# Optimization experiments

Hardware: AMD Instinct MI355X
Metric: run time of the kernel (lower is better)

Reference implementation:

```python
import jax, jax.numpy as jnp
import numpy as np

N, M, NBR = 20000, 12, 64
AF, ORIG, H, B, K = 256, 92, 256, 200, 50
N_CONV = 3
EPS = 1e-5


def _bn_train(x, gamma, beta):
    mu = x.mean(0)
    var = x.var(0)  # biased, matches torch BN normalization in train mode
    return (x - mu) * jax.lax.rsqrt(var + EPS) * gamma + beta


def _conv_layer(atom_in, nbr_fea, nbr_idx, w1, b1, w2, b2, gamma, beta):
    n, m = nbr_idx.shape
    m1 = m // 2
    atom_nbr = atom_in[nbr_idx]                     # [N, M, AF]
    atom_u = jnp.broadcast_to(atom_in[:, None, :], (n, m1, atom_in.shape[-1]))
    an1, an2 = atom_nbr[:, :m1], atom_nbr[:, m1:]
    nf1, nf2 = nbr_fea[:, :m1], nbr_fea[:, m1:]
    u1 = jnp.concatenate([atom_u, an1, nf1], axis=2)  # [N, M1, 2*AF+NBR]
    u2 = jnp.concatenate([atom_u, an2, nf2], axis=2)
    g1 = jax.nn.relu(jnp.einsum('nmf,fo->nmo', u1, w1) + b1)
    g2 = jax.nn.softplus(jnp.einsum('nmf,fo->nmo', u2, w1) + b1)
    nbr_sumed = g1.sum(1) + g2.sum(1)               # sum over all M neighbors, [N, 2*AF]
    nbr_sumed = nbr_sumed @ w2 + b2                 # [N, AF]
    nbr_sumed = _bn_train(nbr_sumed, gamma, beta)
    return jax.nn.softplus(atom_in + nbr_sumed)


def setup_inputs() -> dict:
    key = jax.random.key(0)
    ks = jax.random.split(key, 16)
    inp = {
        'atom_fea': jax.random.normal(ks[0], (N, ORIG), jnp.float32),
        'nbr_fea': jax.random.normal(ks[1], (N, M, NBR), jnp.float32),
        'nbr_fea_idx': jax.random.randint(ks[2], (N, M), 0, N),
        'M1_index': jax.random.randint(ks[3], (B * K,), 0, N),
        'seg_ids': jnp.repeat(jnp.arange(B), K),
        'm2_fea': jax.random.normal(ks[4], (B, 4), jnp.float32),
        'emb_w': jax.random.normal(ks[5], (ORIG, AF), jnp.float32) * 0.05,
        'emb_b': jnp.zeros((AF,), jnp.float32),
        'w1': jax.random.normal(ks[6], (N_CONV, 2 * AF + NBR, 2 * AF), jnp.float32) * 0.05,
        'b1': jnp.zeros((N_CONV, 2 * AF), jnp.float32),
        'w2': jax.random.normal(ks[7], (N_CONV, 2 * AF, AF), jnp.float32) * 0.05,
        'b2': jnp.zeros((N_CONV, AF), jnp.float32),
        'gamma': jnp.ones((N_CONV, AF), jnp.float32),
        'beta': jnp.zeros((N_CONV, AF), jnp.float32),
        'fc_w': jax.random.normal(ks[8], (AF + 4, H), jnp.float32) * 0.05,
        'fc_b': jnp.zeros((H,), jnp.float32),
        'out_w': jax.random.normal(ks[9], (H, 1), jnp.float32) * 0.05,
        'out_b': jnp.zeros((1,), jnp.float32),
    }
    return inp


def reference(atom_fea, nbr_fea, nbr_fea_idx, M1_index, seg_ids, m2_fea,
              emb_w, emb_b, w1, b1, w2, b2, gamma, beta,
              fc_w, fc_b, out_w, out_b):
    x = jax.nn.softplus(atom_fea @ emb_w + emb_b)           # [N, AF]
    for i in range(N_CONV):
        x = _conv_layer(x, nbr_fea, nbr_fea_idx, w1[i], b1[i], w2[i], b2[i], gamma[i], beta[i])
    m1_fea = x[M1_index]                                    # [B*K, AF]
    sums = jax.ops.segment_sum(m1_fea, seg_ids, num_segments=B)
    counts = jax.ops.segment_sum(jnp.ones((m1_fea.shape[0], 1), m1_fea.dtype), seg_ids, num_segments=B)
    crys = sums / counts                                    # per-crystal mean, [B, AF]
    crys = jnp.concatenate([crys, m2_fea], axis=1)          # [B, AF+4]
    h = jax.nn.softplus(jax.nn.softplus(crys) @ fc_w + fc_b)
    out = h @ out_w + out_b                                 # [B, 1]
    return out
```

## Files before the change

### kernel.cpp

```cpp
#include <hip/hip_runtime.h>
#include <hip/hip_bf16.h>


#define N_ATOM 20000
#define AF     256
#define F2     512
#define ORIG   92
#define ORIG_P 96
#define BB     200
#define KK     50
#define BN_EPS 1e-5f
#define ZPS    132

#define OFF_B1   0
#define OFF_B2   1536
#define OFF_GAM  2304
#define OFF_BET  3072
#define OFF_EMBB 3840
#define OFF_FCB  4096
#define OFF_FCW  4352
#define OFF_OW   70912
#define OFF_OB   71168
#define OFF_M2   71169
#define N_SMALL  71969

#define S_AF   (N_ATOM * ORIG_P)
#define S_EMB  (AF * ORIG_P)
#define S_W12  (3 * 1024 * 256)
#define S_W1F  (3 * 512 * 64)
#define S_W2   (3 * AF * F2)
#define S_SM   N_SMALL
#define S_TOT  (S_AF + S_EMB + S_W12 + S_W1F + S_W2 + S_SM)

using bf16x8 = __attribute__((ext_vector_type(8))) short;
using f32x4  = __attribute__((ext_vector_type(4))) float;

__device__ __forceinline__ float bf2f(__hip_bfloat16 v) { return __bfloat162float(v); }
__device__ __forceinline__ __hip_bfloat16 f2bf(float v) { return __float2bfloat16(v); }
__device__ __forceinline__ unsigned short f2bfbits(float f) {
    unsigned u = __float_as_uint(f);
    u += 0x7fffu + ((u >> 16) & 1u);
    return (unsigned short)(u >> 16);
}
__device__ __forceinline__ float bfbits2f(unsigned short u) {
    return __uint_as_float(((unsigned)u) << 16);
}
__device__ __forceinline__ unsigned pack2bf(float lo, float hi) {
    unsigned ul = __float_as_uint(lo);
    unsigned uh = __float_as_uint(hi);
    ul += 0x7fffu + ((ul >> 16) & 1u);
    uh += 0x7fffu + ((uh >> 16) & 1u);
    return __builtin_amdgcn_perm(uh, ul, 0x07060302u);
}
__device__ __forceinline__ float softplus_f(float x) {
    return fmaxf(x, 0.f) + __logf(1.f + __expf(-fabsf(x)));
}
__device__ __forceinline__ float ld_any(const void* p, long idx, bool isf32) {
    return isf32 ? ((const float*)p)[idx] : bf2f(((const __hip_bfloat16*)p)[idx]);
}

__global__ void detect_dtype(const unsigned* __restrict__ gamma_raw,
                             unsigned* __restrict__ flag) {
    unsigned u = gamma_raw[0];
    flag[0] = ((u & 0xFFFFu) == 0u) ? 1u : 0u;
}

__global__ __launch_bounds__(256) void prep_nf(const void* __restrict__ nf,
                                               const unsigned* __restrict__ dflag,
                                               unsigned* __restrict__ out) {
    bool isf32 = dflag[0] != 0u;
    int idx = blockIdx.x * 256 + threadIdx.x;
    if (idx >= N_ATOM * 12 * 64 / 4) return;
    if (isf32) {
        float4 v = ((const float4*)nf)[idx];
        out[idx * 2]     = pack2bf(v.x, v.y);
        out[idx * 2 + 1] = pack2bf(v.z, v.w);
    } else {
        ((uint2*)out)[idx] = ((const uint2*)nf)[idx];
    }
}

__global__ __launch_bounds__(256)
void prep_all(const void* af, const void* emb_w, const void* w1, const void* w2,
              const void* b1, const void* b2, const void* gam, const void* bet,
              const void* embb, const void* fcb, const void* fcw,
              const void* ow, const void* ob, const void* m2,
              const unsigned* __restrict__ dflag,
              __hip_bfloat16* __restrict__ af_pad, __hip_bfloat16* __restrict__ embT,
              __hip_bfloat16* __restrict__ w1T2, __hip_bfloat16* __restrict__ w1Tf,
              __hip_bfloat16* __restrict__ w2T, __hip_bfloat16* __restrict__ smalls) {
    bool isf32 = dflag[0] != 0u;
    int i = blockIdx.x * 256 + threadIdx.x;
    if (i < S_AF) {
        int r = i / ORIG_P, k = i - r * ORIG_P;
        af_pad[i] = (k < ORIG) ? f2bf(ld_any(af, (long)r * ORIG + k, isf32)) : f2bf(0.f);
        return;
    }
    i -= S_AF;
    if (i < S_EMB) {
        int n = i / ORIG_P, k = i - n * ORIG_P;
        embT[i] = (k < ORIG) ? f2bf(ld_any(emb_w, (long)k * AF + n, isf32)) : f2bf(0.f);
        return;
    }
    i -= S_EMB;
    if (i < S_W12) {
        int l = i / (1024 * 256); int rem = i - l * (1024 * 256);
        int c = rem / 256, k = rem - c * 256;
        long src = (c < 512) ? ((long)(l * 576 + k) * F2 + c)
                             : ((long)(l * 576 + 256 + k) * F2 + (c - 512));
        w1T2[i] = f2bf(ld_any(w1, src, isf32));
        return;
    }
    i -= S_W12;
    if (i < S_W1F) {
        int l = i / (512 * 64); int rem = i - l * (512 * 64);
        int c = rem / 64, k = rem - c * 64;
        w1Tf[i] = f2bf(ld_any(w1, (long)(l * 576 + 512 + k) * F2 + c, isf32));
        return;
    }
    i -= S_W1F;
    if (i < S_W2) {
        int l = i / (AF * F2); int rem = i - l * (AF * F2);
        int n = rem / F2, k = rem - n * F2;
        w2T[i] = f2bf(ld_any(w2, (long)(l * F2 + k) * AF + n, isf32));
        return;
    }
    i -= S_W2;
    if (i >= S_SM) return;
    float v;
    if      (i < OFF_B2)   v = ld_any(b1,   i - OFF_B1,  isf32);
    else if (i < OFF_GAM)  v = ld_any(b2,   i - OFF_B2,  isf32);
    else if (i < OFF_BET)  v = ld_any(gam,  i - OFF_GAM, isf32);
    else if (i < OFF_EMBB) v = ld_any(bet,  i - OFF_BET, isf32);
    else if (i < OFF_FCB)  v = ld_any(embb, i - OFF_EMBB,isf32);
    else if (i < OFF_OW)   v = (i < OFF_FCW) ? ld_any(fcb, i - OFF_FCB, isf32)
                                             : ld_any(fcw, i - OFF_FCW, isf32);
    else if (i < OFF_OB)   v = ld_any(ow,   i - OFF_OW,  isf32);
    else if (i < OFF_M2)   v = ld_any(ob,   i - OFF_OB,  isf32);
    else                   v = ld_any(m2,   i - OFF_M2,  isf32);
    smalls[i] = f2bf(v);
}

template <bool OUT_BF16>
__global__ __launch_bounds__(256)
void gemm_kernel(const __hip_bfloat16* __restrict__ A, int lda,
                 const __hip_bfloat16* __restrict__ BT, int ldb,
                 void* __restrict__ Cp, int M, int ldc, int K,
                 const __hip_bfloat16* __restrict__ bias, int act,
                 float* __restrict__ st) {
    __shared__ __align__(16) unsigned short sA[128 * 40];
    __shared__ __align__(16) unsigned short sB[128 * 40];
    __shared__ float sS[128], sS2[128];
    int tid  = threadIdx.x;
    int mt   = blockIdx.x, nt = blockIdx.y;
    int wave = tid >> 6, lane = tid & 63, q = lane >> 4, ln = lane & 15;
    int wr   = wave >> 1, wc = wave & 1;

    if (st && tid < 128) { sS[tid] = 0.f; sS2[tid] = 0.f; }

    f32x4 acc[4][4];
    for (int i = 0; i < 4; i++)
        for (int j = 0; j < 4; j++) acc[i][j] = (f32x4){0.f, 0.f, 0.f, 0.f};

    for (int k0 = 0; k0 < K; k0 += 32) {
        for (int i = tid; i < 512; i += 256) {
            int r = i >> 2, ch = i & 3;
            int row = mt * 128 + r;
            uint4 va = make_uint4(0u, 0u, 0u, 0u);
            if (row < M) va = *(const uint4*)(A + (size_t)row * lda + k0 + ch * 8);
            *(uint4*)(&sA[r * 40 + ch * 8]) = va;
            int n = nt * 128 + r;
            uint4 vb = *(const uint4*)(BT + (size_t)n * ldb + k0 + ch * 8);
            *(uint4*)(&sB[r * 40 + ch * 8]) = vb;
        }
        __syncthreads();
        bf16x8 af[4], bf[4];
        for (int i = 0; i < 4; i++)
            af[i] = *(const bf16x8*)(&sA[(wr * 64 + i * 16 + ln) * 40 + q * 8]);
        for (int j = 0; j < 4; j++)
            bf[j] = *(const bf16x8*)(&sB[(wc * 64 + j * 16 + ln) * 40 + q * 8]);
        for (int i = 0; i < 4; i++)
            for (int j = 0; j < 4; j++)
                acc[i][j] = __builtin_amdgcn_mfma_f32_16x16x32_bf16(af[i], bf[j], acc[i][j], 0, 0, 0);
        __syncthreads();
    }
    for (int j = 0; j < 4; j++) {
        int cl  = wc * 64 + j * 16 + ln;
        int col = nt * 128 + cl;
        float bv = bias ? bf2f(bias[col]) : 0.f;
        float ls = 0.f, ls2 = 0.f;
        for (int i = 0; i < 4; i++) {
            for (int r = 0; r < 4; r++) {
                int row = mt * 128 + wr * 64 + i * 16 + q * 4 + r;
                if (row >= M) continue;
                float v = acc[i][j][r] + bv;
                if (st) { ls += v; ls2 += v * v; }
                if (act == 1) v = softplus_f(v);
                if (OUT_BF16) ((__hip_bfloat16*)Cp)[(size_t)row * ldc + col] = f2bf(v);
                else          ((float*)Cp)[(size_t)row * ldc + col] = v;
            }
        }
        if (st) { atomicAdd(&sS[cl], ls); atomicAdd(&sS2[cl], ls2); }
    }
    if (st) {
        __syncthreads();
        if (tid < 128) {
            int col = nt * 128 + tid;
            atomicAdd(&st[col], sS[tid]);
            atomicAdd(&st[AF + col], sS2[tid]);
        }
    }
}

__global__ __launch_bounds__(256, 5)
void conv_fused(const void* __restrict__ nf,
                const unsigned* __restrict__ dflag,
                int prepped,
                const int* __restrict__ nidx,
                const __hip_bfloat16* __restrict__ xay,
                const __hip_bfloat16* __restrict__ b1l,
                const __hip_bfloat16* __restrict__ w1TfL,
                __hip_bfloat16* __restrict__ ns)
{
    __shared__ __align__(16) unsigned short sNF[48 * 72];
    __shared__ __align__(16) unsigned       sZp[48 * ZPS];
    __shared__ int sIdx[48];

    int tid = threadIdx.x;
    int ab  = blockIdx.x * 4;

    if (prepped || dflag[0] == 0u) {
        const __hip_bfloat16* nfB = (const __hip_bfloat16*)nf;
        for (int i = tid; i < 48 * 8; i += 256) {
            int r = i >> 3, ch = i & 7;
            uint4 v = *(const uint4*)(nfB + (size_t)(ab * 12 + r) * 64 + ch * 8);
            *(uint4*)(&sNF[r * 72 + ch * 8]) = v;
        }
    } else {
        const float* nfF = (const float*)nf;
        for (int i = tid; i < 48 * 8; i += 256) {
            int r = i >> 3, ch = i & 7;
            const float* src = nfF + (size_t)(ab * 12 + r) * 64 + ch * 8;
            float4 v0 = *(const float4*)(src);
            float4 v1 = *(const float4*)(src + 4);
            unsigned* d = (unsigned*)&sNF[r * 72 + ch * 8];
            d[0] = pack2bf(v0.x, v0.y);
            d[1] = pack2bf(v0.z, v0.w);
            d[2] = pack2bf(v1.x, v1.y);
            d[3] = pack2bf(v1.z, v1.w);
        }
    }
    if (tid < 48) sIdx[tid] = nidx[ab * 12 + tid];
    __syncthreads();

    int wave = tid >> 6, lane = tid & 63, q = lane >> 4, ln = lane & 15;
    int c0  = wave * 32;
    int c0h = wave * 16;
    int a = wave, n = ab + a;

    int j5    = lane & 31, c2sel = lane >> 5;
    int t2r   = (j5 >> 4) & 1, wr2 = (j5 >> 2) & 3, lb = j5 & 3;
    int ub    = t2r * 64 + wr2 * 16 + lb * 4;
    int gcp   = t2r * 128 + wr2 * 32 + c2sel * 16 + lb * 4;
    unsigned sel = c2sel ? 0x03020c0cu : 0x01000c0cu;

    unsigned offm[12];
#pragma unroll
    for (int m = 0; m < 12; m++)
        offm[m] = ((unsigned)sIdx[a * 12 + m] << 11) + 1024u;

    for (int tp = 0; tp < 2; tp++) {
        if (tp) __syncthreads();
        for (int t2 = 0; t2 < 2; t2++) {
            int cb = (tp * 2 + t2) * 128;
            bf16x8 bfr[2][2];
            for (int c2 = 0; c2 < 2; c2++)
                for (int ks = 0; ks < 2; ks++)
                    bfr[c2][ks] = *(const bf16x8*)(w1TfL +
                        (size_t)(cb + c0 + c2 * 16 + ln) * 64 + ks * 32 + q * 8);
            f32x4 acc[3][2];
            for (int rt = 0; rt < 3; rt++)
                for (int c2 = 0; c2 < 2; c2++) acc[rt][c2] = (f32x4){0.f, 0.f, 0.f, 0.f};
            for (int rt = 0; rt < 3; rt++) {
                bf16x8 a0 = *(const bf16x8*)(&sNF[(rt * 16 + ln) * 72 + q * 8]);
                bf16x8 a1 = *(const bf16x8*)(&sNF[(rt * 16 + ln) * 72 + 32 + q * 8]);
                acc[rt][0] = __builtin_amdgcn_mfma_f32_16x16x32_bf16(a0, bfr[0][0], acc[rt][0], 0, 0, 0);
                acc[rt][0] = __builtin_amdgcn_mfma_f32_16x16x32_bf16(a1, bfr[0][1], acc[rt][0], 0, 0, 0);
                acc[rt][1] = __builtin_amdgcn_mfma_f32_16x16x32_bf16(a0, bfr[1][0], acc[rt][1], 0, 0, 0);
                acc[rt][1] = __builtin_amdgcn_mfma_f32_16x16x32_bf16(a1, bfr[1][1], acc[rt][1], 0, 0, 0);
            }
#pragma unroll
            for (int rt = 0; rt < 3; rt++)
#pragma unroll
                for (int r = 0; r < 4; r++)
                    sZp[(rt * 16 + q * 4 + r) * ZPS + t2 * 64 + c0h + ln] =
                        pack2bf(acc[rt][0][r], acc[rt][1][r]);
        }
        __syncthreads();

        int gc = tp * 256 + gcp;
        uint2 yy[12];
#pragma unroll
        for (int m = 0; m < 12; m++)
            yy[m] = *(const uint2*)((const char*)xay + offm[m] + gc * 2);
        uint2 xau = *(const uint2*)(xay + (size_t)n * 1024 + gc);
        uint2 b1u = *(const uint2*)(b1l + gc);
        float xa0 = bfbits2f((unsigned short)(xau.x & 0xffff)) +
                    bfbits2f((unsigned short)(b1u.x & 0xffff));
        float xa1 = bfbits2f((unsigned short)(xau.x >> 16)) +
                    bfbits2f((unsigned short)(b1u.x >> 16));
        float xa2 = bfbits2f((unsigned short)(xau.y & 0xffff)) +
                    bfbits2f((unsigned short)(b1u.y & 0xffff));
        float xa3 = bfbits2f((unsigned short)(xau.y >> 16)) +
                    bfbits2f((unsigned short)(b1u.y >> 16));
        float r0 = 0.f, r1 = 0.f, r2 = 0.f, r3 = 0.f;
#pragma unroll
        for (int m = 0; m < 12; m++) {
            uint4 zz = *(const uint4*)(&sZp[(a * 12 + m) * ZPS + ub]);
            float v0 = __uint_as_float(__builtin_amdgcn_perm(zz.x, zz.x, sel)) + xa0 +
                       __uint_as_float(yy[m].x << 16);
            float v1 = __uint_as_float(__builtin_amdgcn_perm(zz.y, zz.y, sel)) + xa1 +
                       __uint_as_float(yy[m].x & 0xffff0000u);
            float v2 = __uint_as_float(__builtin_amdgcn_perm(zz.z, zz.z, sel)) + xa2 +
                       __uint_as_float(yy[m].y << 16);
            float v3 = __uint_as_float(__builtin_amdgcn_perm(zz.w, zz.w, sel)) + xa3 +
                       __uint_as_float(yy[m].y & 0xffff0000u);
            if (m < 6) {
                v0 = fmaxf(v0, 0.f); v1 = fmaxf(v1, 0.f);
                v2 = fmaxf(v2, 0.f); v3 = fmaxf(v3, 0.f);
            } else {
                v0 = softplus_f(v0); v1 = softplus_f(v1);
                v2 = softplus_f(v2); v3 = softplus_f(v3);
            }
            r0 += v0; r1 += v1; r2 += v2; r3 += v3;
        }
        uint2 o;
        o.x = pack2bf(r0, r1);
        o.y = pack2bf(r2, r3);
        *(uint2*)(ns + (size_t)n * F2 + gc) = o;
    }
}

__global__ __launch_bounds__(256)
void bn_apply(const __hip_bfloat16* __restrict__ h2, const float* __restrict__ st,
              const __hip_bfloat16* __restrict__ x,
              const __hip_bfloat16* __restrict__ gamma,
              const __hip_bfloat16* __restrict__ beta,
              __hip_bfloat16* __restrict__ xo) {
    int i = (blockIdx.x * 256 + threadIdx.x) * 8;
    int c = i & 255;
    uint4 hv = *(const uint4*)(h2 + i);
    uint4 xv = *(const uint4*)(x + i);
    unsigned hw[4] = {hv.x, hv.y, hv.z, hv.w};
    unsigned xw[4] = {xv.x, xv.y, xv.z, xv.w};
    unsigned ow[4];
    float r[8];
#pragma unroll
    for (int k = 0; k < 8; k++) {
        int cc = c + k;
        float mu  = st[cc] * (1.f / 20000.f);
        float var = fmaxf(st[AF + cc] * (1.f / 20000.f) - mu * mu, 0.f);
        unsigned hh = hw[k >> 1], xx = xw[k >> 1];
        float h  = bfbits2f((unsigned short)((k & 1) ? (hh >> 16) : (hh & 0xffff)));
        float xf = bfbits2f((unsigned short)((k & 1) ? (xx >> 16) : (xx & 0xffff)));
        float t = (h - mu) * rsqrtf(var + BN_EPS) * bf2f(gamma[cc]) + bf2f(beta[cc]);
        r[k] = softplus_f(xf + t);
    }
#pragma unroll
    for (int k = 0; k < 4; k++)
        ow[k] = pack2bf(r[2 * k], r[2 * k + 1]);
    *(uint4*)(xo + i) = make_uint4(ow[0], ow[1], ow[2], ow[3]);
}

__global__ __launch_bounds__(256)
void readout(const __hip_bfloat16* __restrict__ x, const int* __restrict__ m1,
             const __hip_bfloat16* __restrict__ smalls,
             const unsigned* __restrict__ dflag,
             void* __restrict__ outp) {
    __shared__ float sc[AF + 4];
    __shared__ float sred[4];
    bool isf32 = dflag[0] != 0u;
    int b = blockIdx.x, tid = threadIdx.x;
    float s = 0.f;
    for (int j = 0; j < KK; j++) {
        int row = m1[b * KK + j];
        s += bf2f(x[(size_t)row * AF + tid]);
    }
    sc[tid] = softplus_f(s * (1.f / (float)KK));
    if (tid < 4) sc[AF + tid] = softplus_f(bf2f(smalls[OFF_M2 + b * 4 + tid]));
    __syncthreads();
    float acc = bf2f(smalls[OFF_FCB + tid]);
    for (int k = 0; k < AF + 4; k++) acc += sc[k] * bf2f(smalls[OFF_FCW + k * 256 + tid]);
    float h = softplus_f(acc);
    float v = h * bf2f(smalls[OFF_OW + tid]);
    for (int off = 32; off > 0; off >>= 1) v += __shfl_down(v, off);
    if ((tid & 63) == 0) sred[tid >> 6] = v;
    __syncthreads();
    if (tid == 0) {
        float o = sred[0] + sred[1] + sred[2] + sred[3] + bf2f(smalls[OFF_OB]);
        if (isf32) ((float*)outp)[b] = o;
        else       ((__hip_bfloat16*)outp)[b] = f2bf(o);
    }
}

extern "C" void kernel_launch(void* const* d_in, const int* in_sizes, int n_in,
                              void* d_out, int out_size, void* d_ws, size_t ws_size,
                              hipStream_t stream) {
    const void* atom_fea = d_in[0];
    const void* nbr_fea  = d_in[1];
    const int*  nbr_idx  = (const int*)d_in[2];
    const int*  m1_idx   = (const int*)d_in[3];
    const void* m2_fea = d_in[5];
    const void* emb_w  = d_in[6];
    const void* emb_b  = d_in[7];
    const void* w1     = d_in[8];
    const void* b1     = d_in[9];
    const void* w2     = d_in[10];
    const void* b2     = d_in[11];
    const void* gamma  = d_in[12];
    const void* beta   = d_in[13];
    const void* fc_w   = d_in[14];
    const void* fc_b   = d_in[15];
    const void* out_w  = d_in[16];
    const void* out_b  = d_in[17];

    char* ws = (char*)d_ws;
    size_t off = 0;
    auto alloc = [&](size_t bytes) -> char* {
        char* p = ws + off;
        off += (bytes + 255) & ~(size_t)255;
        return p;
    };
    __hip_bfloat16* w1T2   = (__hip_bfloat16*)alloc((size_t)S_W12 * 2);
    __hip_bfloat16* w1Tf   = (__hip_bfloat16*)alloc((size_t)S_W1F * 2);
    __hip_bfloat16* w2T    = (__hip_bfloat16*)alloc((size_t)S_W2 * 2);
    __hip_bfloat16* smalls = (__hip_bfloat16*)alloc((size_t)N_SMALL * 2);
    __hip_bfloat16* xb0    = (__hip_bfloat16*)alloc((size_t)N_ATOM * AF * 2);
    __hip_bfloat16* xb1    = (__hip_bfloat16*)alloc((size_t)N_ATOM * AF * 2);
    char*           regXY  = alloc((size_t)N_ATOM * 1024 * 2);
    char*           regZ   = alloc((size_t)N_ATOM * F2 * 2);
    float*          stats  = (float*)alloc((size_t)3 * 2 * AF * 4);
    unsigned*       dflag  = (unsigned*)alloc(256);
    char*           nfb    = alloc((size_t)N_ATOM * 12 * 64 * 2);
    int use_nfb = (ws_size >= off) ? 1 : 0;

    __hip_bfloat16* xay    = (__hip_bfloat16*)regXY;
    __hip_bfloat16* h2     = (__hip_bfloat16*)regXY;
    __hip_bfloat16* af_pad = (__hip_bfloat16*)(regXY + (size_t)N_ATOM * F2 * 2);
    __hip_bfloat16* embT   = (__hip_bfloat16*)regZ;
    __hip_bfloat16* nsb    = (__hip_bfloat16*)regZ;

    detect_dtype<<<1, 1, 0, stream>>>((const unsigned*)gamma, dflag);
    (void)hipMemsetAsync(stats, 0, (size_t)3 * 2 * AF * 4, stream);

    if (use_nfb)
        prep_nf<<<(N_ATOM * 12 * 64 / 4 + 255) / 256, 256, 0, stream>>>(nbr_fea, dflag,
                                                                        (unsigned*)nfb);
    prep_all<<<(S_TOT + 255) / 256, 256, 0, stream>>>(
        atom_fea, emb_w, w1, w2, b1, b2, gamma, beta, emb_b, fc_b, fc_w,
        out_w, out_b, m2_fea, dflag, af_pad, embT, w1T2, w1Tf, w2T, smalls);

    dim3 g_emb((N_ATOM + 127) / 128, 2);
    gemm_kernel<true><<<g_emb, 256, 0, stream>>>(af_pad, ORIG_P, embT, ORIG_P,
                                                 xb0, N_ATOM, AF, ORIG_P,
                                                 smalls + OFF_EMBB, 1, nullptr);

    const void* nf_conv = use_nfb ? (const void*)nfb : nbr_fea;

    __hip_bfloat16* xc = xb0;
    __hip_bfloat16* xn = xb1;
    for (int l = 0; l < 3; l++) {
        dim3 gxy((N_ATOM + 127) / 128, 8);
        gemm_kernel<true><<<gxy, 256, 0, stream>>>(xc, AF, w1T2 + (size_t)l * 1024 * 256, 256,
                                                   xay, N_ATOM, 1024, AF, nullptr, 0, nullptr);
        conv_fused<<<N_ATOM / 4, 256, 0, stream>>>(nf_conv, dflag, use_nfb, nbr_idx, xay,
                                                   smalls + OFF_B1 + l * F2,
                                                   w1Tf + (size_t)l * 512 * 64, nsb);
        float* stl = stats + l * 2 * AF;
        dim3 gh2((N_ATOM + 127) / 128, 2);
        gemm_kernel<true><<<gh2, 256, 0, stream>>>(nsb, F2, w2T + (size_t)l * AF * F2, F2,
                                                   h2, N_ATOM, AF, F2,
                                                   smalls + OFF_B2 + l * AF, 0, stl);
        bn_apply<<<(N_ATOM * AF / 8) / 256, 256, 0, stream>>>(h2, stl, xc,
                                                              smalls + OFF_GAM + l * AF,
                                                              smalls + OFF_BET + l * AF, xn);
        __hip_bfloat16* t = xc; xc = xn; xn = t;
    }
    readout<<<BB, 256, 0, stream>>>(xc, m1_idx, smalls, dflag, d_out);
}
```

Baseline: 607.6 us.

## Use direct global-to-LDS loads in GEMM and stream neighbor rows in conv

```diff
diff --git a/kernel.cpp b/kernel.cpp
--- a/kernel.cpp
+++ b/kernel.cpp
@@ -3,6 +3,7 @@
 
 
 #define N_ATOM 20000
+#define N_PAD  20096
 #define AF     256
 #define F2     512
 #define ORIG   92
@@ -148,8 +149,8 @@
                  void* __restrict__ Cp, int M, int ldc, int K,
                  const __hip_bfloat16* __restrict__ bias, int act,
                  float* __restrict__ st) {
-    __shared__ __align__(16) unsigned short sA[128 * 40];
-    __shared__ __align__(16) unsigned short sB[128 * 40];
+    __shared__ __align__(16) unsigned short sA[128 * 32];
+    __shared__ __align__(16) unsigned short sB[128 * 32];
     __shared__ float sS[128], sS2[128];
     int tid  = threadIdx.x;
     int mt   = blockIdx.x, nt = blockIdx.y;
@@ -163,22 +164,27 @@
         for (int j = 0; j < 4; j++) acc[i][j] = (f32x4){0.f, 0.f, 0.f, 0.f};
 
     for (int k0 = 0; k0 < K; k0 += 32) {
-        for (int i = tid; i < 512; i += 256) {
-            int r = i >> 2, ch = i & 3;
-            int row = mt * 128 + r;
-            uint4 va = make_uint4(0u, 0u, 0u, 0u);
-            if (row < M) va = *(const uint4*)(A + (size_t)row * lda + k0 + ch * 8);
-            *(uint4*)(&sA[r * 40 + ch * 8]) = va;
-            int n = nt * 128 + r;
-            uint4 vb = *(const uint4*)(BT + (size_t)n * ldb + k0 + ch * 8);
-            *(uint4*)(&sB[r * 40 + ch * 8]) = vb;
+        const __hip_bfloat16* Ab = A + (size_t)mt * 128 * lda + k0;
+        const __hip_bfloat16* Bb = BT + (size_t)nt * 128 * ldb + k0;
+#pragma unroll
+        for (int j = 0; j < 2; j++) {
+            int idx = j * 256 + tid;
+            int r = idx >> 2, ch = idx & 3;
+            __builtin_amdgcn_global_load_lds(
+                (const __attribute__((address_space(1))) void*)(Ab + (size_t)r * lda + ch * 8),
+                (__attribute__((address_space(3))) void*)(sA + (j * 256 + wave * 64) * 8),
+                16, 0, 0);
+            __builtin_amdgcn_global_load_lds(
+                (const __attribute__((address_space(1))) void*)(Bb + (size_t)r * ldb + ch * 8),
+                (__attribute__((address_space(3))) void*)(sB + (j * 256 + wave * 64) * 8),
+                16, 0, 0);
         }
         __syncthreads();
         bf16x8 af[4], bf[4];
         for (int i = 0; i < 4; i++)
-            af[i] = *(const bf16x8*)(&sA[(wr * 64 + i * 16 + ln) * 40 + q * 8]);
+            af[i] = *(const bf16x8*)(&sA[(wr * 64 + i * 16 + ln) * 32 + q * 8]);
         for (int j = 0; j < 4; j++)
-            bf[j] = *(const bf16x8*)(&sB[(wc * 64 + j * 16 + ln) * 40 + q * 8]);
+            bf[j] = *(const bf16x8*)(&sB[(wc * 64 + j * 16 + ln) * 32 + q * 8]);
         for (int i = 0; i < 4; i++)
             for (int j = 0; j < 4; j++)
                 acc[i][j] = __builtin_amdgcn_mfma_f32_16x16x32_bf16(af[i], bf[j], acc[i][j], 0, 0, 0);
@@ -212,7 +218,7 @@
     }
 }
 
-__global__ __launch_bounds__(256, 5)
+__global__ __launch_bounds__(256)
 void conv_fused(const void* __restrict__ nf,
                 const unsigned* __restrict__ dflag,
                 int prepped,
@@ -299,10 +305,7 @@
         __syncthreads();
 
         int gc = tp * 256 + gcp;
-        uint2 yy[12];
-#pragma unroll
-        for (int m = 0; m < 12; m++)
-            yy[m] = *(const uint2*)((const char*)xay + offm[m] + gc * 2);
+        unsigned gc2 = (unsigned)gc * 2;
         uint2 xau = *(const uint2*)(xay + (size_t)n * 1024 + gc);
         uint2 b1u = *(const uint2*)(b1l + gc);
         float xa0 = bfbits2f((unsigned short)(xau.x & 0xffff)) +
@@ -316,15 +319,16 @@
         float r0 = 0.f, r1 = 0.f, r2 = 0.f, r3 = 0.f;
 #pragma unroll
         for (int m = 0; m < 12; m++) {
+            uint2 yv = *(const uint2*)((const char*)xay + offm[m] + gc2);
             uint4 zz = *(const uint4*)(&sZp[(a * 12 + m) * ZPS + ub]);
             float v0 = __uint_as_float(__builtin_amdgcn_perm(zz.x, zz.x, sel)) + xa0 +
-                       __uint_as_float(yy[m].x << 16);
+                       __uint_as_float(yv.x << 16);
             float v1 = __uint_as_float(__builtin_amdgcn_perm(zz.y, zz.y, sel)) + xa1 +
-                       __uint_as_float(yy[m].x & 0xffff0000u);
+                       __uint_as_float(yv.x & 0xffff0000u);
             float v2 = __uint_as_float(__builtin_amdgcn_perm(zz.z, zz.z, sel)) + xa2 +
-                       __uint_as_float(yy[m].y << 16);
+                       __uint_as_float(yv.y << 16);
             float v3 = __uint_as_float(__builtin_amdgcn_perm(zz.w, zz.w, sel)) + xa3 +
-                       __uint_as_float(yy[m].y & 0xffff0000u);
+                       __uint_as_float(yv.y & 0xffff0000u);
             if (m < 6) {
                 v0 = fmaxf(v0, 0.f); v1 = fmaxf(v1, 0.f);
                 v2 = fmaxf(v2, 0.f); v3 = fmaxf(v3, 0.f);
@@ -435,10 +439,10 @@
     __hip_bfloat16* w1Tf   = (__hip_bfloat16*)alloc((size_t)S_W1F * 2);
     __hip_bfloat16* w2T    = (__hip_bfloat16*)alloc((size_t)S_W2 * 2);
     __hip_bfloat16* smalls = (__hip_bfloat16*)alloc((size_t)N_SMALL * 2);
-    __hip_bfloat16* xb0    = (__hip_bfloat16*)alloc((size_t)N_ATOM * AF * 2);
-    __hip_bfloat16* xb1    = (__hip_bfloat16*)alloc((size_t)N_ATOM * AF * 2);
+    __hip_bfloat16* xb0    = (__hip_bfloat16*)alloc((size_t)N_PAD * AF * 2);
+    __hip_bfloat16* xb1    = (__hip_bfloat16*)alloc((size_t)N_PAD * AF * 2);
     char*           regXY  = alloc((size_t)N_ATOM * 1024 * 2);
-    char*           regZ   = alloc((size_t)N_ATOM * F2 * 2);
+    char*           regZ   = alloc((size_t)N_PAD * F2 * 2);
     float*          stats  = (float*)alloc((size_t)3 * 2 * AF * 4);
     unsigned*       dflag  = (unsigned*)alloc(256);
     char*           nfb    = alloc((size_t)N_ATOM * 12 * 64 * 2);
```

Result: faster. 594.7 us (-2.1%).
